# Kernel tuning notes

Measured on AMD Instinct MI355X. Metric: run time of the kernel, lower is better.

The kernel has to match this reference:

```python
import jax, jax.numpy as jnp
from jax import lax
import numpy as np

B, N = 512, 256
INF = jnp.float32(1e30)


def setup_inputs() -> dict:
    key = jax.random.key(0)
    k1, k2 = jax.random.split(key)
    costs = jax.random.normal(k1, (B, N, N), dtype=jnp.float32)
    pad_mask = jax.random.randint(k2, (B, N), 0, 2).astype(bool)
    return {"costs": costs, "pad_mask": pad_mask}


def _solve_lap(cost):
    """Jonker-Volgenant shortest-augmenting-path LAP, same math as
    scipy.optimize.linear_sum_assignment. cost: [n, n], rows=objects,
    cols=predictions. Returns col4row[n]: assigned column per row."""
    n = cost.shape[0]
    idx = jnp.arange(n, dtype=jnp.int32)

    def assign_row(cur_row, state):
        u, v, col4row, row4col = state
        cur_row = jnp.int32(cur_row)

        def path_cond(c):
            return c[2] < 0

        def path_body(c):
            i, minval, sink, shortest, pathrow, SR, SC = c
            SR = SR.at[i].set(True)
            r = minval + cost[i] - u[i] - v  # reduced cost of extending path via row i
            upd = jnp.logical_and(~SC, r < shortest)
            shortest = jnp.where(upd, r, shortest)
            pathrow = jnp.where(upd, i, pathrow)
            masked = jnp.where(SC, INF, shortest)
            j = jnp.argmin(masked).astype(jnp.int32)
            minval = masked[j]
            SC = SC.at[j].set(True)
            nxt = row4col[j]
            sink = jnp.where(nxt < 0, j, jnp.int32(-1))
            i = jnp.where(nxt < 0, i, nxt)
            return (i, minval, sink, shortest, pathrow, SR, SC)

        init = (cur_row, jnp.float32(0.0), jnp.int32(-1),
                jnp.full((n,), INF, jnp.float32),
                jnp.full((n,), -1, jnp.int32),
                jnp.zeros((n,), bool), jnp.zeros((n,), bool))
        i, minval, sink, shortest, pathrow, SR, SC = lax.while_loop(
            path_cond, path_body, init)

        # dual updates (Crouse 2016 / scipy lsap)
        u = u.at[cur_row].add(minval)
        others = jnp.logical_and(SR, idx != cur_row)
        u = u + jnp.where(others, minval - shortest[jnp.clip(col4row, 0, n - 1)], 0.0)
        v = v - jnp.where(SC, minval - shortest, 0.0)

        # augment along the alternating path back to cur_row
        def aug_cond(c):
            return ~c[3]

        def aug_body(c):
            j, col4row, row4col, done = c
            i = pathrow[j]
            row4col = row4col.at[j].set(i)
            j_next = col4row[i]
            col4row = col4row.at[i].set(j)
            return (j_next, col4row, row4col, i == cur_row)

        _, col4row, row4col, _ = lax.while_loop(
            aug_cond, aug_body, (sink, col4row, row4col, jnp.bool_(False)))
        return (u, v, col4row, row4col)

    state = (jnp.zeros((n,), jnp.float32), jnp.zeros((n,), jnp.float32),
             jnp.full((n,), -1, jnp.int32), jnp.full((n,), -1, jnp.int32))
    _, _, col4row, _ = lax.fori_loop(0, n, assign_row, state)
    return col4row


def _match_one(cost_t, n_k):
    # cost_t: [n_obj_slots, n_pred] (== costs[k].T); n_k: number of valid objects
    n = cost_t.shape[0]
    idx = jnp.arange(n, dtype=jnp.int32)
    rows_valid = idx < n_k
    # padded object rows get constant cost -> assignment of real rows unchanged
    P = jnp.where(rows_valid[:, None], cost_t, 0.0)
    cols = _solve_lap(P)
    # prediction indices used by real objects (cols is a permutation)
    used = jnp.zeros((n,), bool).at[cols].set(rows_valid)
    # unused prediction indices, ascending, placed first
    order = jnp.argsort(jnp.where(used, idx + n, idx)).astype(jnp.int32)
    fill = order[jnp.clip(idx - n_k, 0, n - 1)]
    return jnp.where(rows_valid, cols, fill)


def _forward(costs, pad_mask):
    costs = jnp.nan_to_num(costs.astype(jnp.float32),
                           nan=1e6, posinf=1e6, neginf=1e6)
    n_k = jnp.sum(pad_mask, axis=1).astype(jnp.int32)  # valid objects per batch
    cost_t = jnp.swapaxes(costs, 1, 2)                 # [B, n_obj, n_pred]
    return jax.vmap(_match_one)(cost_t, n_k)


def reference(costs, pad_mask):
    return _forward(costs, pad_mask)
```

## Files before the change

### kernel.cpp

```cpp
#include <hip/hip_runtime.h>
#include <math.h>

#define NB 512
#define NN 256
#define NCACHE 60
#define LAP_INF 1e30f

#define WS_NK_OFF 1024
#define WS_PT_OFF 8192

__global__ __launch_bounds__(1024)
void detect_kernel(const unsigned int* __restrict__ pw, int* __restrict__ flag) {
  __shared__ int notInt, notFloat;
  if (threadIdx.x == 0) { notInt = 0; notFloat = 0; }
  __syncthreads();
  int li = 0, lf = 0;
  for (int t = threadIdx.x; t < 32768; t += 1024) {
    unsigned int w = pw[t];
    if (w > 1u) li = 1;
    if (w != 0u && w != 0x3F800000u) lf = 1;
  }
  if (li) atomicOr(&notInt, 1);
  if (lf) atomicOr(&notFloat, 1);
  __syncthreads();
  if (threadIdx.x == 0) flag[0] = (!notInt) ? 1 : ((!notFloat) ? 2 : 0);
}

__global__ __launch_bounds__(64)
void nk_kernel(const void* __restrict__ pm, const int* __restrict__ flag,
               int* __restrict__ nk) {
  const int k = blockIdx.x;
  const int lane = threadIdx.x;
  const int fl = flag[0];
  int cnt4 = 0;
  if (fl == 1) {
    const int* p = ((const int*)pm) + k * NN;
#pragma unroll
    for (int q = 0; q < 4; ++q) cnt4 += (p[lane * 4 + q] != 0);
  } else if (fl == 2) {
    const float* p = ((const float*)pm) + k * NN;
#pragma unroll
    for (int q = 0; q < 4; ++q) cnt4 += (p[lane * 4 + q] != 0.0f);
  } else {
    const unsigned char* p = ((const unsigned char*)pm) + k * NN;
#pragma unroll
    for (int q = 0; q < 4; ++q) cnt4 += (p[lane * 4 + q] != 0);
  }
#pragma unroll
  for (int off = 32; off > 0; off >>= 1) cnt4 += __shfl_down(cnt4, off);
  if (lane == 0) nk[k] = cnt4;
}

__global__ __launch_bounds__(256)
void transpose_kernel(const float* __restrict__ in, float* __restrict__ out,
                      const int* __restrict__ nk) {
  const int k = blockIdx.z;
  const int i0 = blockIdx.x * 32;
  int bnd = nk[k];
  bnd = bnd > NCACHE ? bnd : NCACHE;
  if (i0 >= bnd) return;
  __shared__ float tile[32][33];
  const float* A = in + ((size_t)k << 16);
  float* Bp = out + ((size_t)k << 16);
  const int tx = threadIdx.x, ty = threadIdx.y;
  const int j0 = blockIdx.y * 32;
#pragma unroll
  for (int r = 0; r < 32; r += 8) {
    float x = A[(size_t)(j0 + ty + r) * NN + (i0 + tx)];
    tile[ty + r][tx] = isfinite(x) ? x : 1e6f;
  }
  __syncthreads();
#pragma unroll
  for (int r = 0; r < 32; r += 8) {
    Bp[(size_t)(i0 + ty + r) * NN + (j0 + tx)] = tile[tx][ty + r];
  }
}

template <int CTRL>
__device__ __forceinline__ unsigned dpp_min_step(unsigned x) {
  unsigned y = (unsigned)__builtin_amdgcn_update_dpp((int)x, (int)x, CTRL, 0xF, 0xF, false);
  return y < x ? y : x;
}
__device__ __forceinline__ unsigned wave_min_u32(unsigned x) {
  x = dpp_min_step<0xB1>(x);
  x = dpp_min_step<0x4E>(x);
  x = dpp_min_step<0x141>(x);
  x = dpp_min_step<0x140>(x);
  x = dpp_min_step<0x142>(x);
  x = dpp_min_step<0x143>(x);
  return (unsigned)__builtin_amdgcn_readlane((int)x, 63);
}
__device__ __forceinline__ unsigned f2o(float f) {
  unsigned x = __float_as_uint(f);
  return x ^ ((unsigned)((int)x >> 31) | 0x80000000u);
}
__device__ __forceinline__ float o2f(unsigned m) {
  unsigned x = (m & 0x80000000u) ? (m & 0x7FFFFFFFu) : ~m;
  return __uint_as_float(x);
}
__device__ __forceinline__ int sel4(const int a[4], int s) {
  return (s == 0) ? a[0] : (s == 1) ? a[1] : (s == 2) ? a[2] : a[3];
}
__device__ __forceinline__ void set4(int a[4], int s, int v) {
  if (s == 0) a[0] = v; else if (s == 1) a[1] = v;
  else if (s == 2) a[2] = v; else a[3] = v;
}
__device__ __forceinline__ void setf4(float a[4], int s, float v) {
  if (s == 0) a[0] = v; else if (s == 1) a[1] = v;
  else if (s == 2) a[2] = v; else a[3] = v;
}

__global__ __launch_bounds__(64)
void lap_kernel(const float* __restrict__ costs, const void* __restrict__ pm,
                const int* __restrict__ flag, const int* __restrict__ nkArr,
                const float* __restrict__ Pt, int* __restrict__ out, int useT) {
  const int k = blockIdx.x;
  const int lane = threadIdx.x;

  __shared__ __align__(16) float rowCache[NCACHE][NN];
  __shared__ float shortestL[NN];
  __shared__ int freeRowsL[NN];
  __shared__ unsigned char used[NN];

  const float* PtK = Pt + ((size_t)k << 16);
  const float* costK = costs + ((size_t)k << 16);

  int n_k;
  if (useT) {
    n_k = nkArr[k];
  } else {
    const int fl = flag[0];
    int cnt4 = 0;
    if (fl == 1) {
      const int* p = ((const int*)pm) + k * NN;
#pragma unroll
      for (int q = 0; q < 4; ++q) cnt4 += (p[lane * 4 + q] != 0);
    } else if (fl == 2) {
      const float* p = ((const float*)pm) + k * NN;
#pragma unroll
      for (int q = 0; q < 4; ++q) cnt4 += (p[lane * 4 + q] != 0.0f);
    } else {
      const unsigned char* p = ((const unsigned char*)pm) + k * NN;
#pragma unroll
      for (int q = 0; q < 4; ++q) cnt4 += (p[lane * 4 + q] != 0);
    }
#pragma unroll
    for (int off = 32; off > 0; off >>= 1) cnt4 += __shfl_down(cnt4, off);
    n_k = __shfl(cnt4, 0);
  }

  if (useT) {
    const float4* s4 = (const float4*)PtK;
    float4* c4 = (float4*)rowCache;
    for (int t = lane; t < NCACHE * (NN / 4); t += 64) c4[t] = s4[t];
  } else {
    for (int e = lane; e < NCACHE * NN; e += 64) {
      const int i = e >> 8, j = e & 255;
      float x = costK[(size_t)j * NN + i];
      rowCache[i][j] = isfinite(x) ? x : 1e6f;
    }
  }

  float vv[4] = {0.f, 0.f, 0.f, 0.f};
  float uu[4] = {0.f, 0.f, 0.f, 0.f};
  int r4c[4] = {-1, -1, -1, -1};
  int c4r[4] = {-1, -1, -1, -1};
  int nfree = 0;
  __syncthreads();

  float4 carry = {0.f, 0.f, 0.f, 0.f};
  for (int r = 0; r < n_k; ++r) {
    float cc[4];
    if (r < NCACHE) {
      const float4 rv = *(const float4*)(&rowCache[r][lane * 4]);
      cc[0] = rv.x; cc[1] = rv.y; cc[2] = rv.z; cc[3] = rv.w;
    } else if (useT) {
      cc[0] = carry.x; cc[1] = carry.y; cc[2] = carry.z; cc[3] = carry.w;
    } else {
#pragma unroll
      for (int q = 0; q < 4; ++q) {
        float x = costK[(size_t)(lane * 4 + q) * NN + r];
        cc[q] = isfinite(x) ? x : 1e6f;
      }
    }
    if (useT && r + 1 >= NCACHE && r + 1 < n_k)
      carry = *(const float4*)(PtK + (size_t)(r + 1) * NN + lane * 4);

    unsigned lbv = 0xFFFFFFFFu;
    int lbq = 0;
#pragma unroll
    for (int q = 0; q < 4; ++q) {
      const unsigned m = f2o(cc[q]);
      if (m < lbv) { lbv = m; lbq = q; }
    }
    const unsigned gv = wave_min_u32(lbv);
    const unsigned long long cmask = __ballot(lbv == gv);
    const int owner = __ffsll((unsigned long long)cmask) - 1;
    const int js = (owner << 2) + __builtin_amdgcn_readlane(lbq, owner);
    if (lane == (r >> 2)) setf4(uu, r & 3, o2f(gv));
    const int occ = __builtin_amdgcn_readlane(sel4(r4c, js & 3), owner);
    if (occ < 0) {
      if (lane == owner) set4(r4c, js & 3, r);
      if (lane == (r >> 2)) set4(c4r, r & 3, js);
    } else {
      if (lane == 0) freeRowsL[nfree] = r;
      nfree++;
    }
  }
  __syncthreads();

  for (int t = 0; t < nfree; ++t) {
    const int cur = freeRowsL[t];
    float sh[4] = {LAP_INF, LAP_INF, LAP_INF, LAP_INF};
    int pr[4] = {-1, -1, -1, -1};
    unsigned scm = 0;
    unsigned srm = 0;
    float minval = 0.f;
    int i = cur, sink = -1;

    while (sink < 0) {
      const int islot = i & 3, iowner = i >> 2;
      if (lane == iowner) srm |= (1u << islot);
      const float su = (islot == 0) ? uu[0] : (islot == 1) ? uu[1]
                     : (islot == 2) ? uu[2] : uu[3];
      const float ui = __int_as_float(
          __builtin_amdgcn_readlane(__float_as_int(su), iowner));

      float cc[4];
      if (i < NCACHE) {
        const float4 rv = *(const float4*)(&rowCache[i][lane * 4]);
        cc[0] = rv.x; cc[1] = rv.y; cc[2] = rv.z; cc[3] = rv.w;
      } else if (useT) {
        const float4 rv = *(const float4*)(PtK + (size_t)i * NN + lane * 4);
        cc[0] = rv.x; cc[1] = rv.y; cc[2] = rv.z; cc[3] = rv.w;
      } else {
#pragma unroll
        for (int q = 0; q < 4; ++q) {
          float x = costK[(size_t)(lane * 4 + q) * NN + i];
          cc[q] = isfinite(x) ? x : 1e6f;
        }
      }

      unsigned lbv = 0xFFFFFFFFu;
      int lbq = 0;
#pragma unroll
      for (int q = 0; q < 4; ++q) {
        float r = minval + cc[q];
        r = r - ui;
        r = r - vv[q];
        const bool sc = (scm >> q) & 1u;
        if (!sc && r < sh[q]) { sh[q] = r; pr[q] = i; }
        const unsigned m = sc ? 0xFFFFFFFFu : f2o(sh[q]);
        if (m < lbv) { lbv = m; lbq = q; }
      }
      const unsigned gv = wave_min_u32(lbv);
      minval = o2f(gv);
      const unsigned long long cmask = __ballot(lbv == gv);
      const int owner = __ffsll((unsigned long long)cmask) - 1;
      const int js = (owner << 2) + __builtin_amdgcn_readlane(lbq, owner);
      if (lane == owner) scm |= (1u << lbq);
      const int nxt = __builtin_amdgcn_readlane(sel4(r4c, js & 3), owner);
      if (nxt < 0) sink = js; else i = nxt;
    }

#pragma unroll
    for (int q = 0; q < 4; ++q) shortestL[lane * 4 + q] = sh[q];
    __syncthreads();

#pragma unroll
    for (int q = 0; q < 4; ++q) {
      if ((srm >> q) & 1u) {
        const int row = lane * 4 + q;
        if (row == cur) uu[q] = uu[q] + minval;
        else uu[q] = uu[q] + (minval - shortestL[c4r[q]]);
      }
      if ((scm >> q) & 1u) vv[q] = vv[q] - (minval - sh[q]);
    }

    int j = sink;
    bool done = false;
    while (!done) {
      const int pi = __builtin_amdgcn_readlane(sel4(pr, j & 3), j >> 2);
      if (lane == (j >> 2)) set4(r4c, j & 3, pi);
      const int jn = __builtin_amdgcn_readlane(sel4(c4r, pi & 3), pi >> 2);
      if (lane == (pi >> 2)) set4(c4r, pi & 3, j);
      done = (pi == cur);
      j = jn;
    }
    __syncthreads();
  }

  for (int t = lane; t < NN; t += 64) used[t] = 0;
  __syncthreads();
#pragma unroll
  for (int q = 0; q < 4; ++q) {
    const int row = lane * 4 + q;
    if (row < n_k) used[c4r[q]] = 1;
  }
  __syncthreads();
  int* outK = out + k * NN;
#pragma unroll
  for (int q = 0; q < 4; ++q) {
    const int row = lane * 4 + q;
    if (row < n_k) outK[row] = c4r[q];
  }
  if (lane == 0) {
    int pos = n_k;
    for (int c = 0; c < NN; ++c)
      if (!used[c]) outK[pos++] = c;
  }
}

extern "C" void kernel_launch(void* const* d_in, const int* in_sizes, int n_in,
                              void* d_out, int out_size, void* d_ws, size_t ws_size,
                              hipStream_t stream) {
  const float* costs = (const float*)d_in[0];
  const void* pm = d_in[1];
  int* out = (int*)d_out;

  int* flag = (int*)d_ws;
  int* nk = (int*)((char*)d_ws + WS_NK_OFF);
  float* Pt = (float*)((char*)d_ws + WS_PT_OFF);
  const size_t need = WS_PT_OFF + (size_t)NB * NN * NN * sizeof(float);
  const int useT = (ws_size >= need) ? 1 : 0;

  detect_kernel<<<1, 1024, 0, stream>>>((const unsigned int*)pm, flag);
  nk_kernel<<<NB, 64, 0, stream>>>(pm, flag, nk);
  if (useT) {
    dim3 g(8, 8, NB), b(32, 8);
    transpose_kernel<<<g, b, 0, stream>>>(costs, Pt, nk);
  }
  lap_kernel<<<NB, 64, 0, stream>>>(costs, pm, flag, nk, useT ? Pt : costs,
                                    out, useT);
}
```

Measured before the change: 412.2 us.

## Precompute per-row minima in a parallel kernel before the serial LAP init

Adds a rowmin_kernel that computes each row's minimum value and argmin across many blocks. The LAP kernel then reads these results to initialise the row duals and the greedy column assignment, instead of scanning every row serially inside one wave per batch. The goal is to take the serial per-row reduction off the critical path of the single-wave LAP blocks. In exchange it adds a kernel launch, needs extra workspace (falling back to the old path when workspace is small), and adds global traffic for the row minima.

```diff
diff --git a/kernel.cpp b/kernel.cpp
--- a/kernel.cpp
+++ b/kernel.cpp
@@ -7,7 +7,10 @@
 #define LAP_INF 1e30f
 
 #define WS_NK_OFF 1024
-#define WS_PT_OFF 8192
+#define WS_RMV_OFF 8192
+#define WS_RMA_OFF (8192 + 512 * 1024)
+#define WS_PT_OFF_FULL (8192 + 1024 * 1024)
+#define WS_PT_OFF_R4 8192
 
 __global__ __launch_bounds__(1024)
 void detect_kernel(const unsigned int* __restrict__ pw, int* __restrict__ flag) {
@@ -110,10 +113,36 @@
   else if (s == 2) a[2] = v; else a[3] = v;
 }
 
+__global__ __launch_bounds__(256)
+void rowmin_kernel(const float* __restrict__ Pt, const int* __restrict__ nk,
+                   float* __restrict__ rmv, int* __restrict__ rma) {
+  const int k = blockIdx.x;
+  const int wid = threadIdx.x >> 6, lane = threadIdx.x & 63;
+  const int row = blockIdx.y * 4 + wid;
+  int bnd = nk[k];
+  bnd = bnd > NCACHE ? bnd : NCACHE;
+  if (row >= bnd) return;
+  const float4 rv = *(const float4*)(Pt + ((size_t)k << 16) + (size_t)row * NN + lane * 4);
+  float bv = rv.x; int bj = lane * 4;
+  if (rv.y < bv) { bv = rv.y; bj = lane * 4 + 1; }
+  if (rv.z < bv) { bv = rv.z; bj = lane * 4 + 2; }
+  if (rv.w < bv) { bv = rv.w; bj = lane * 4 + 3; }
+  const unsigned m = f2o(bv);
+  const unsigned g = wave_min_u32(m);
+  const unsigned long long cm = __ballot(m == g);
+  const int owner = __ffsll(cm) - 1;
+  const int ja = __builtin_amdgcn_readlane(bj, owner);
+  if (lane == 0) {
+    rmv[k * NN + row] = o2f(g);
+    rma[k * NN + row] = ja;
+  }
+}
+
 __global__ __launch_bounds__(64)
 void lap_kernel(const float* __restrict__ costs, const void* __restrict__ pm,
                 const int* __restrict__ flag, const int* __restrict__ nkArr,
-                const float* __restrict__ Pt, int* __restrict__ out, int useT) {
+                const float* __restrict__ rmv, const int* __restrict__ rma,
+                const float* __restrict__ Pt, int* __restrict__ out, int mode) {
   const int k = blockIdx.x;
   const int lane = threadIdx.x;
 
@@ -126,7 +155,7 @@
   const float* costK = costs + ((size_t)k << 16);
 
   int n_k;
-  if (useT) {
+  if (mode >= 1) {
     n_k = nkArr[k];
   } else {
     const int fl = flag[0];
@@ -149,7 +178,7 @@
     n_k = __shfl(cnt4, 0);
   }
 
-  if (useT) {
+  if (mode >= 1) {
     const float4* s4 = (const float4*)PtK;
     float4* c4 = (float4*)rowCache;
     for (int t = lane; t < NCACHE * (NN / 4); t += 64) c4[t] = s4[t];
@@ -165,46 +194,68 @@
   float uu[4] = {0.f, 0.f, 0.f, 0.f};
   int r4c[4] = {-1, -1, -1, -1};
   int c4r[4] = {-1, -1, -1, -1};
+  int ja[4] = {-1, -1, -1, -1};
   int nfree = 0;
   __syncthreads();
 
-  float4 carry = {0.f, 0.f, 0.f, 0.f};
-  for (int r = 0; r < n_k; ++r) {
-    float cc[4];
-    if (r < NCACHE) {
-      const float4 rv = *(const float4*)(&rowCache[r][lane * 4]);
-      cc[0] = rv.x; cc[1] = rv.y; cc[2] = rv.z; cc[3] = rv.w;
-    } else if (useT) {
-      cc[0] = carry.x; cc[1] = carry.y; cc[2] = carry.z; cc[3] = carry.w;
-    } else {
+  if (mode == 2) {
+    const float4 mv = *(const float4*)(rmv + k * NN + lane * 4);
+    const int4 av = *(const int4*)(rma + k * NN + lane * 4);
+    uu[0] = mv.x; uu[1] = mv.y; uu[2] = mv.z; uu[3] = mv.w;
+    ja[0] = av.x; ja[1] = av.y; ja[2] = av.z; ja[3] = av.w;
+#pragma unroll
+    for (int q = 0; q < 4; ++q)
+      if (lane * 4 + q >= n_k) uu[q] = 0.f;
+    for (int r = 0; r < n_k; ++r) {
+      const int js = __builtin_amdgcn_readlane(sel4(ja, r & 3), r >> 2);
+      const int occ = __builtin_amdgcn_readlane(sel4(r4c, js & 3), js >> 2);
+      if (occ < 0) {
+        if (lane == (js >> 2)) set4(r4c, js & 3, r);
+        if (lane == (r >> 2)) set4(c4r, r & 3, js);
+      } else {
+        if (lane == 0) freeRowsL[nfree] = r;
+        nfree++;
+      }
+    }
+  } else {
+    float4 carry = {0.f, 0.f, 0.f, 0.f};
+    for (int r = 0; r < n_k; ++r) {
+      float cc[4];
+      if (r < NCACHE) {
+        const float4 rv = *(const float4*)(&rowCache[r][lane * 4]);
+        cc[0] = rv.x; cc[1] = rv.y; cc[2] = rv.z; cc[3] = rv.w;
+      } else if (mode >= 1) {
+        cc[0] = carry.x; cc[1] = carry.y; cc[2] = carry.z; cc[3] = carry.w;
+      } else {
+#pragma unroll
+        for (int q = 0; q < 4; ++q) {
+          float x = costK[(size_t)(lane * 4 + q) * NN + r];
+          cc[q] = isfinite(x) ? x : 1e6f;
+        }
+      }
+      if (mode >= 1 && r + 1 >= NCACHE && r + 1 < n_k)
+        carry = *(const float4*)(PtK + (size_t)(r + 1) * NN + lane * 4);
+
+      unsigned lbv = 0xFFFFFFFFu;
+      int lbq = 0;
 #pragma unroll
       for (int q = 0; q < 4; ++q) {
-        float x = costK[(size_t)(lane * 4 + q) * NN + r];
-        cc[q] = isfinite(x) ? x : 1e6f;
-      }
-    }
-    if (useT && r + 1 >= NCACHE && r + 1 < n_k)
-      carry = *(const float4*)(PtK + (size_t)(r + 1) * NN + lane * 4);
-
-    unsigned lbv = 0xFFFFFFFFu;
-    int lbq = 0;
-#pragma unroll
-    for (int q = 0; q < 4; ++q) {
-      const unsigned m = f2o(cc[q]);
-      if (m < lbv) { lbv = m; lbq = q; }
-    }
-    const unsigned gv = wave_min_u32(lbv);
-    const unsigned long long cmask = __ballot(lbv == gv);
-    const int owner = __ffsll((unsigned long long)cmask) - 1;
-    const int js = (owner << 2) + __builtin_amdgcn_readlane(lbq, owner);
-    if (lane == (r >> 2)) setf4(uu, r & 3, o2f(gv));
-    const int occ = __builtin_amdgcn_readlane(sel4(r4c, js & 3), owner);
-    if (occ < 0) {
-      if (lane == owner) set4(r4c, js & 3, r);
-      if (lane == (r >> 2)) set4(c4r, r & 3, js);
-    } else {
-      if (lane == 0) freeRowsL[nfree] = r;
-      nfree++;
+        const unsigned m = f2o(cc[q]);
+        if (m < lbv) { lbv = m; lbq = q; }
+      }
+      const unsigned gv = wave_min_u32(lbv);
+      const unsigned long long cmask = __ballot(lbv == gv);
+      const int owner = __ffsll((unsigned long long)cmask) - 1;
+      const int js = (owner << 2) + __builtin_amdgcn_readlane(lbq, owner);
+      if (lane == (r >> 2)) setf4(uu, r & 3, o2f(gv));
+      const int occ = __builtin_amdgcn_readlane(sel4(r4c, js & 3), owner);
+      if (occ < 0) {
+        if (lane == owner) set4(r4c, js & 3, r);
+        if (lane == (r >> 2)) set4(c4r, r & 3, js);
+      } else {
+        if (lane == 0) freeRowsL[nfree] = r;
+        nfree++;
+      }
     }
   }
   __syncthreads();
@@ -230,7 +281,7 @@
       if (i < NCACHE) {
         const float4 rv = *(const float4*)(&rowCache[i][lane * 4]);
         cc[0] = rv.x; cc[1] = rv.y; cc[2] = rv.z; cc[3] = rv.w;
-      } else if (useT) {
+      } else if (mode >= 1) {
         const float4 rv = *(const float4*)(PtK + (size_t)i * NN + lane * 4);
         cc[0] = rv.x; cc[1] = rv.y; cc[2] = rv.z; cc[3] = rv.w;
       } else {
@@ -320,16 +371,34 @@
 
   int* flag = (int*)d_ws;
   int* nk = (int*)((char*)d_ws + WS_NK_OFF);
-  float* Pt = (float*)((char*)d_ws + WS_PT_OFF);
-  const size_t need = WS_PT_OFF + (size_t)NB * NN * NN * sizeof(float);
-  const int useT = (ws_size >= need) ? 1 : 0;
+  const size_t ptBytes = (size_t)NB * NN * NN * sizeof(float);
+
+  int mode;
+  float* rmv; int* rma; float* Pt;
+  if (ws_size >= WS_PT_OFF_FULL + ptBytes) {
+    mode = 2;
+    rmv = (float*)((char*)d_ws + WS_RMV_OFF);
+    rma = (int*)((char*)d_ws + WS_RMA_OFF);
+    Pt = (float*)((char*)d_ws + WS_PT_OFF_FULL);
+  } else if (ws_size >= WS_PT_OFF_R4 + ptBytes) {
+    mode = 1;
+    rmv = (float*)d_ws; rma = (int*)d_ws;
+    Pt = (float*)((char*)d_ws + WS_PT_OFF_R4);
+  } else {
+    mode = 0;
+    rmv = (float*)d_ws; rma = (int*)d_ws;
+    Pt = (float*)costs;
+  }
 
   detect_kernel<<<1, 1024, 0, stream>>>((const unsigned int*)pm, flag);
   nk_kernel<<<NB, 64, 0, stream>>>(pm, flag, nk);
-  if (useT) {
+  if (mode >= 1) {
     dim3 g(8, 8, NB), b(32, 8);
     transpose_kernel<<<g, b, 0, stream>>>(costs, Pt, nk);
   }
-  lap_kernel<<<NB, 64, 0, stream>>>(costs, pm, flag, nk, useT ? Pt : costs,
-                                    out, useT);
-}
+  if (mode == 2) {
+    dim3 g(NB, 64);
+    rowmin_kernel<<<g, 256, 0, stream>>>(Pt, nk, rmv, rma);
+  }
+  lap_kernel<<<NB, 64, 0, stream>>>(costs, pm, flag, nk, rmv, rma, Pt, out, mode);
+}
```

Result: no change. 406.6 us (-1.3%).
